# Performance work log

Measured on AMD Instinct MI355X. Metric: run time of the kernel, lower is better.

Reference implementation:

```python
import jax, jax.numpy as jnp
import numpy as np

B, S, D, H = 2, 2048, 1024, 16
DK = D // H
DFF = 4 * D
EPS = 1e-6


def layer_norm(x, gamma, beta):
    mu = jnp.mean(x, axis=-1, keepdims=True)
    var = jnp.mean(jnp.square(x - mu), axis=-1, keepdims=True)
    return (x - mu) * jax.lax.rsqrt(var + EPS) * gamma + beta


def setup_inputs() -> dict:
    key = jax.random.key(0)
    ks = jax.random.split(key, 10)
    xavier = (6.0 / (D + D)) ** 0.5
    kaiming = (6.0 / D) ** 0.5
    kaiming2 = (6.0 / DFF) ** 0.5
    return {
        "batch_X": jax.random.normal(ks[0], (B, S, D), dtype=jnp.float32),
        "padding_mask": jax.random.randint(ks[1], (B, S), 0, 2, dtype=jnp.int32),
        "W_Q": jax.random.uniform(ks[2], (D, D), jnp.float32, -xavier, xavier),
        "W_K": jax.random.uniform(ks[3], (D, D), jnp.float32, -xavier, xavier),
        "W_V": jax.random.uniform(ks[4], (D, D), jnp.float32, -xavier, xavier),
        "W_O": jax.random.uniform(ks[5], (D, D), jnp.float32, -xavier, xavier),
        "W1": jax.random.uniform(ks[6], (D, DFF), jnp.float32, -kaiming, kaiming),
        "b1": jnp.zeros((DFF,), jnp.float32),
        "W2": jax.random.uniform(ks[7], (DFF, D), jnp.float32, -kaiming2, kaiming2),
        "b2": jnp.zeros((D,), jnp.float32),
        "gamma1": jnp.ones((D,), jnp.float32),
        "beta1": jnp.zeros((D,), jnp.float32),
        "gamma2": jnp.ones((D,), jnp.float32),
        "beta2": jnp.zeros((D,), jnp.float32),
    }


def reference(batch_X, padding_mask, W_Q, W_K, W_V, W_O, W1, b1, W2, b2,
              gamma1, beta1, gamma2, beta2):
    x = batch_X
    b, s, d = x.shape

    # --- multi-head self-attention (use_mask=False: padding mask only) ---
    q = (x @ W_Q).reshape(b, s, H, DK)
    k = (x @ W_K).reshape(b, s, H, DK)
    v = (x @ W_V).reshape(b, s, H, DK)
    scores = jnp.einsum("bqhd,bkhd->bhqk", q, k) / jnp.sqrt(jnp.float32(DK))
    # mask[b,i,j] = (padding_mask[b,i] == 0) for all j: whole query rows are
    # either fully masked (softmax -> NaN -> zeroed in the original) or
    # fully unmasked. Equivalent math: softmax then zero padded query rows.
    probs = jax.nn.softmax(scores, axis=-1)
    keep = (padding_mask != 0).astype(probs.dtype)[:, None, :, None]  # [B,1,S,1]
    probs = probs * keep
    ctx = jnp.einsum("bhqk,bkhd->bqhd", probs, v).reshape(b, s, d)
    attn_out = ctx @ W_O

    # --- residual + LN (dropout identity in eval) ---
    x = x + layer_norm(attn_out, gamma1, beta1)

    # --- FFN ---
    h = jax.nn.relu(x @ W1 + b1)
    ffn_out = h @ W2 + b2
    x = x + layer_norm(ffn_out, gamma2, beta2)
    return x
```

## Files before the change

kernel.cpp:

```cpp
#include <hip/hip_runtime.h>

#define B 2
#define S 2048
#define D 1024
#define H 16
#define DKh 64
#define DFF 4096
#define M (B*S)

typedef unsigned short u16;
typedef unsigned int u32;
typedef __attribute__((ext_vector_type(8))) short short8;
typedef __attribute__((ext_vector_type(4))) float f32x4;

__device__ __forceinline__ u16 f2bf(float f) {
  union { float f; unsigned u; } v; v.f = f;
  unsigned r = v.u + 0x7fffu + ((v.u >> 16) & 1u);
  return (u16)(r >> 16);
}

__device__ __forceinline__ u32 pkbf(float a, float b) {
  union { float f; u32 u; } ua, ub; ua.f = a; ub.f = b;
  return ((ub.u + 0x8000u) & 0xffff0000u) | ((ua.u + 0x8000u) >> 16);
}

__device__ __forceinline__ void gload16(const void* g, void* l) {
  __builtin_amdgcn_global_load_lds((const __attribute__((address_space(1))) void*)g,
                                   (__attribute__((address_space(3))) void*)l, 16, 0, 0);
}

__global__ __launch_bounds__(256) void cvtbf(const float* __restrict__ in,
                                             u16* __restrict__ out, int n4) {
  int i = blockIdx.x * 256 + threadIdx.x;
  if (i >= n4) return;
  float4 v = ((const float4*)in)[i];
  ushort4 o = make_ushort4(f2bf(v.x), f2bf(v.y), f2bf(v.z), f2bf(v.w));
  ((ushort4*)out)[i] = o;
}

__global__ __launch_bounds__(256) void tcvt(const float* __restrict__ W,
                                            u16* __restrict__ Wt, int K, int N) {
  __shared__ u16 l[64][65];
  const int n0 = blockIdx.x * 64, k0 = blockIdx.y * 64;
  const int tx = threadIdx.x & 63, ty = threadIdx.x >> 6;
#pragma unroll
  for (int j = 0; j < 16; ++j) {
    int r = j * 4 + ty;
    l[r][tx] = f2bf(W[(size_t)(k0 + r) * N + n0 + tx]);
  }
  __syncthreads();
#pragma unroll
  for (int j = 0; j < 16; ++j) {
    int r = j * 4 + ty;
    Wt[(size_t)(n0 + r) * K + k0 + tx] = l[tx][r];
  }
}

__global__ __launch_bounds__(256) void vtrans(const u16* __restrict__ V,
                                              u16* __restrict__ Vt, int ld) {
  __shared__ u16 l[64][65];
  const int s0 = blockIdx.x * 64, by = blockIdx.y;
  const int b = by >> 4, h = by & 15;
  const int tx = threadIdx.x & 63, ty = threadIdx.x >> 6;
#pragma unroll
  for (int j = 0; j < 16; ++j) {
    int r = j * 4 + ty;
    l[r][tx] = V[(size_t)(b * S + s0 + r) * ld + h * DKh + tx];
  }
  __syncthreads();
#pragma unroll
  for (int j = 0; j < 16; ++j) {
    int r = j * 4 + ty;
    Vt[(size_t)(by * 64 + r) * S + s0 + tx] = l[tx][r];
  }
}

template<int EPI, int SPLIT2>
__global__ __launch_bounds__(256) void gemm_bt(const u16* __restrict__ A,
    const u16* __restrict__ Bt, void* __restrict__ Cout,
    const float* __restrict__ bias, int Mm, int N, int Kd) {
  __shared__ u16 lA[128 * 32];
  __shared__ u16 lB[128 * 32];
  const int t = threadIdx.x;
  const int lane = t & 63, w = t >> 6;
  const int wm = w >> 1, wn = w & 1;
  const int g = lane >> 4, c = lane & 15;

  const int gx = gridDim.x, gy = gridDim.y;
  const int orig = blockIdx.y * gx + blockIdx.x;
  const int qchunk = (gx * gy) >> 3;
  const int wg = (orig & 7) * qchunk + (orig >> 3);
  const int bn0 = (wg % gx) * 128, bm0 = (wg / gx) * 128;

  const int khalf = SPLIT2 ? (Kd >> 1) : Kd;
  const int koff = SPLIT2 ? blockIdx.z * khalf : 0;
  const int nk = khalf >> 5;
  f32x4 acc[4][4] = {};

  const int srow = t >> 2;
  const int scb = (t & 3) * 8;

  auto stage = [&](int kt) {
    gload16(A + (size_t)(bm0 + srow) * Kd + koff + kt * 32 + scb, (void*)(lA + t * 8));
    gload16(A + (size_t)(bm0 + 64 + srow) * Kd + koff + kt * 32 + scb, (void*)(lA + 2048 + t * 8));
    gload16(Bt + (size_t)(bn0 + srow) * Kd + koff + kt * 32 + scb, (void*)(lB + t * 8));
    gload16(Bt + (size_t)(bn0 + 64 + srow) * Kd + koff + kt * 32 + scb, (void*)(lB + 2048 + t * 8));
  };

  stage(0);
  for (int kt = 0; kt < nk; ++kt) {
    __syncthreads();
    short8 af[4], bfr[4];
#pragma unroll
    for (int mt = 0; mt < 4; ++mt)
      af[mt] = *(const short8*)&lA[(wm * 64 + mt * 16 + c) * 32 + g * 8];
#pragma unroll
    for (int nt = 0; nt < 4; ++nt)
      bfr[nt] = *(const short8*)&lB[(wn * 64 + nt * 16 + c) * 32 + g * 8];
#pragma unroll
    for (int mt = 0; mt < 4; ++mt)
#pragma unroll
      for (int nt = 0; nt < 4; ++nt)
        acc[mt][nt] = __builtin_amdgcn_mfma_f32_16x16x32_bf16(af[mt], bfr[nt], acc[mt][nt], 0, 0, 0);
    __syncthreads();
    if (kt + 1 < nk) stage(kt + 1);
  }

  float* plane = SPLIT2 ? ((float*)Cout + (size_t)blockIdx.z * Mm * N) : (float*)Cout;
#pragma unroll
  for (int mt = 0; mt < 4; ++mt) {
#pragma unroll
    for (int nt = 0; nt < 4; ++nt) {
      const int col = bn0 + wn * 64 + nt * 16 + c;
      float bv = (EPI == 2) ? bias[col] : 0.0f;
#pragma unroll
      for (int r = 0; r < 4; ++r) {
        const int row = bm0 + wm * 64 + mt * 16 + g * 4 + r;
        float v = acc[mt][nt][r];
        if (EPI == 2) v = fmaxf(v + bv, 0.0f);
        if (EPI == 1 || SPLIT2) plane[(size_t)row * N + col] = v;
        else                    ((u16*)Cout)[(size_t)row * N + col] = f2bf(v);
      }
    }
  }
}

__global__ __launch_bounds__(256) void attn_kernel(const u16* __restrict__ Q,
    const u16* __restrict__ Kp, const u16* __restrict__ Vt,
    const int* __restrict__ mask, u16* __restrict__ Ctx, int ldq) {
  __shared__ u16 lK[2][64 * 64];
  __shared__ u16 lV[2][64 * 64];
  __shared__ u16 lP[4 * 16 * 64];
  const int t = threadIdx.x, lane = t & 63, w = t >> 6;
  const int g = lane >> 4, c = lane & 15;
  const int gx = gridDim.x;
  const int orig = blockIdx.y * gx + blockIdx.x;
  const int qchunk = (gx * gridDim.y) >> 3;
  const int wg = (orig & 7) * qchunk + (orig >> 3);
  const int bx = wg % gx, by = wg / gx;
  const int b = by >> 4, h = by & 15;
  const int q0w = bx * 64 + w * 16;
  const float SCL = 0.18033688011112042f;

  short8 qf[2];
#pragma unroll
  for (int kc = 0; kc < 2; ++kc)
    qf[kc] = *(const short8*)&Q[(size_t)(b * S + q0w + c) * ldq + h * DKh + kc * 32 + g * 8];

  float lsum = 0.0f;
  f32x4 accO[4] = {};

  auto stage = [&](int buf, int it) {
    const int kv0 = it * 64;
#pragma unroll
    for (int q = 0; q < 2; ++q) {
      int idx = q * 256 + t;
      int row = idx >> 3;
      int colb = (idx & 7) * 16;
      int scol = colb ^ ((row & 7) << 4);
      gload16(Kp + (size_t)(b * S + kv0 + row) * ldq + h * DKh + scol / 2,
              (void*)(&lK[buf][0] + idx * 8));
      gload16(Vt + (size_t)(by * 64 + row) * S + kv0 + scol / 2,
              (void*)(&lV[buf][0] + idx * 8));
    }
  };

  stage(0, 0);
  int cur = 0;
  for (int it = 0; it < S / 64; ++it) {
    __syncthreads();
    if (it + 1 < S / 64) stage(cur ^ 1, it + 1);

    f32x4 sc[4];
#pragma unroll
    for (int ct = 0; ct < 4; ++ct) {
      f32x4 z = {0.f, 0.f, 0.f, 0.f};
#pragma unroll
      for (int kc = 0; kc < 2; ++kc) {
        int row = ct * 16 + c;
        int bcol = (kc * 64 + g * 16) ^ ((row & 7) << 4);
        short8 kf = *(const short8*)&lK[cur][row * 64 + bcol / 2];
        z = __builtin_amdgcn_mfma_f32_16x16x32_bf16(kf, qf[kc], z, 0, 0, 0);
      }
      sc[ct] = z;
    }

#pragma unroll
    for (int ct = 0; ct < 4; ++ct) {
      float p0 = __builtin_amdgcn_exp2f(sc[ct][0] * SCL);
      float p1 = __builtin_amdgcn_exp2f(sc[ct][1] * SCL);
      float p2 = __builtin_amdgcn_exp2f(sc[ct][2] * SCL);
      float p3 = __builtin_amdgcn_exp2f(sc[ct][3] * SCL);
      lsum += (p0 + p1) + (p2 + p3);
      uint2 pk;
      pk.x = pkbf(p0, p1);
      pk.y = pkbf(p2, p3);
      *(uint2*)&lP[w * 1024 + c * 64 + (((ct * 32 + g * 8) ^ ((c & 7) << 4)) >> 1)] = pk;
    }

    short8 pa[2];
#pragma unroll
    for (int kc = 0; kc < 2; ++kc)
      pa[kc] = *(const short8*)&lP[w * 1024 + c * 64 + (((kc * 64 + g * 16) ^ ((c & 7) << 4)) >> 1)];
#pragma unroll
    for (int dt = 0; dt < 4; ++dt) {
#pragma unroll
      for (int kc = 0; kc < 2; ++kc) {
        int rowV = dt * 16 + c;
        int bcolV = (kc * 64 + g * 16) ^ ((rowV & 7) << 4);
        short8 vb = *(const short8*)&lV[cur][rowV * 64 + bcolV / 2];
        accO[dt] = __builtin_amdgcn_mfma_f32_16x16x32_bf16(pa[kc], vb, accO[dt], 0, 0, 0);
      }
    }
    cur ^= 1;
  }

  lsum += __shfl_xor(lsum, 16);
  lsum += __shfl_xor(lsum, 32);

#pragma unroll
  for (int r = 0; r < 4; ++r) {
    int qrow = g * 4 + r;
    float lq = __shfl(lsum, qrow);
    int q = q0w + qrow;
    int keep = mask[b * S + q];
    float inv = (keep != 0) ? (1.0f / lq) : 0.0f;
#pragma unroll
    for (int dt = 0; dt < 4; ++dt) {
      float o = accO[dt][r] * inv;
      Ctx[(size_t)(b * S + q) * D + h * DKh + dt * 16 + c] = f2bf(o);
    }
  }
}

__global__ __launch_bounds__(256) void ln_res(const float* __restrict__ Y1,
    const float* __restrict__ Y2, const float* __restrict__ bias,
    const float* __restrict__ Xres, const float* __restrict__ gamma,
    const float* __restrict__ beta, float* __restrict__ outF,
    u16* __restrict__ outB) {
  __shared__ float s1[4], s2[4];
  const int row = blockIdx.x, t = threadIdx.x;
  float4 y = ((const float4*)(Y1 + (size_t)row * D))[t];
  if (Y2) {
    const float4 y2 = ((const float4*)(Y2 + (size_t)row * D))[t];
    y.x += y2.x; y.y += y2.y; y.z += y2.z; y.w += y2.w;
  }
  if (bias) {
    const float4 bb = ((const float4*)bias)[t];
    y.x += bb.x; y.y += bb.y; y.z += bb.z; y.w += bb.w;
  }
  float sm = y.x + y.y + y.z + y.w;
  float sq = y.x * y.x + y.y * y.y + y.z * y.z + y.w * y.w;
#pragma unroll
  for (int m2 = 1; m2 <= 32; m2 <<= 1) { sm += __shfl_xor(sm, m2); sq += __shfl_xor(sq, m2); }
  if ((t & 63) == 0) { s1[t >> 6] = sm; s2[t >> 6] = sq; }
  __syncthreads();
  float tot = s1[0] + s1[1] + s1[2] + s1[3];
  float tsq = s2[0] + s2[1] + s2[2] + s2[3];
  float mu = tot * (1.0f / D);
  float var = tsq * (1.0f / D) - mu * mu;
  float rstd = rsqrtf(var + 1e-6f);
  const float4 xr = ((const float4*)(Xres + (size_t)row * D))[t];
  const float4 ga = ((const float4*)gamma)[t];
  const float4 be = ((const float4*)beta)[t];
  float4 o;
  o.x = xr.x + (y.x - mu) * rstd * ga.x + be.x;
  o.y = xr.y + (y.y - mu) * rstd * ga.y + be.y;
  o.z = xr.z + (y.z - mu) * rstd * ga.z + be.z;
  o.w = xr.w + (y.w - mu) * rstd * ga.w + be.w;
  ((float4*)(outF + (size_t)row * D))[t] = o;
  if (outB) {
    ushort4 ob = make_ushort4(f2bf(o.x), f2bf(o.y), f2bf(o.z), f2bf(o.w));
    ((ushort4*)outB)[(size_t)row * (D / 4) + t] = ob;
  }
}

extern "C" void kernel_launch(void* const* d_in, const int* in_sizes, int n_in,
                              void* d_out, int out_size, void* d_ws, size_t ws_size,
                              hipStream_t stream) {
  const float* X   = (const float*)d_in[0];
  const int*   msk = (const int*)d_in[1];
  const float* WQ  = (const float*)d_in[2];
  const float* WK  = (const float*)d_in[3];
  const float* WV  = (const float*)d_in[4];
  const float* WO  = (const float*)d_in[5];
  const float* W1  = (const float*)d_in[6];
  const float* b1  = (const float*)d_in[7];
  const float* W2  = (const float*)d_in[8];
  const float* b2  = (const float*)d_in[9];
  const float* g1  = (const float*)d_in[10];
  const float* be1 = (const float*)d_in[11];
  const float* g2  = (const float*)d_in[12];
  const float* be2 = (const float*)d_in[13];
  float* out = (float*)d_out;

  char* ws = (char*)d_ws;
  size_t off = 0;
  auto alloc = [&](size_t bytes) {
    void* p = ws + off;
    off += (bytes + 1023) & ~(size_t)1023;
    return p;
  };
  u16* Xb     = (u16*)alloc((size_t)M * D * 2);
  u16* WQKVt  = (u16*)alloc((size_t)3 * D * D * 2);
  u16* WOt    = (u16*)alloc((size_t)D * D * 2);
  u16* W1t    = (u16*)alloc((size_t)DFF * D * 2);
  u16* W2t    = (u16*)alloc((size_t)D * DFF * 2);
  u16* QKVb   = (u16*)alloc((size_t)M * 3 * D * 2);
  u16* Vt     = (u16*)alloc((size_t)B * H * DKh * S * 2);
  u16* Ctx    = (u16*)alloc((size_t)M * D * 2);
  float* X1f  = (float*)alloc((size_t)M * D * 4);
  u16* X1b    = (u16*)alloc((size_t)M * D * 2);
  u16* Hb     = (u16*)alloc((size_t)M * DFF * 2);
  float* PP   = (float*)QKVb;
  if (off > ws_size) return;

  dim3 blk(256);

  cvtbf<<<dim3(M * D / 4 / 256), blk, 0, stream>>>(X, Xb, M * D / 4);
  tcvt<<<dim3(D / 64, D / 64), blk, 0, stream>>>(WQ, WQKVt + 0 * D * D, D, D);
  tcvt<<<dim3(D / 64, D / 64), blk, 0, stream>>>(WK, WQKVt + 1 * D * D, D, D);
  tcvt<<<dim3(D / 64, D / 64), blk, 0, stream>>>(WV, WQKVt + 2 * D * D, D, D);
  tcvt<<<dim3(D / 64, D / 64), blk, 0, stream>>>(WO, WOt, D, D);
  tcvt<<<dim3(DFF / 64, D / 64), blk, 0, stream>>>(W1, W1t, D, DFF);
  tcvt<<<dim3(D / 64, DFF / 64), blk, 0, stream>>>(W2, W2t, DFF, D);
  gemm_bt<0, 0><<<dim3(3 * D / 128, M / 128), blk, 0, stream>>>(Xb, WQKVt, QKVb, nullptr, M, 3 * D, D);
  vtrans<<<dim3(S / 64, B * H), blk, 0, stream>>>(QKVb + 2 * D, Vt, 3 * D);
  attn_kernel<<<dim3(S / 64, B * H), blk, 0, stream>>>(QKVb, QKVb + D, Vt, msk, Ctx, 3 * D);
  gemm_bt<1, 1><<<dim3(D / 128, M / 128, 2), blk, 0, stream>>>(Ctx, WOt, PP, nullptr, M, D, D);
  ln_res<<<dim3(M), blk, 0, stream>>>(PP, PP + (size_t)M * D, nullptr, X, g1, be1, X1f, X1b);
  gemm_bt<2, 0><<<dim3(DFF / 128, M / 128), blk, 0, stream>>>(X1b, W1t, Hb, b1, M, DFF, D);
  gemm_bt<1, 1><<<dim3(D / 128, M / 128, 2), blk, 0, stream>>>(Hb, W2t, PP, nullptr, M, D, DFF);
  ln_res<<<dim3(M), blk, 0, stream>>>(PP, PP + (size_t)M * D, b2, X1f, g2, be2, out, nullptr);
}
```

Baseline: 296.3 us.

## Replace 128x128 GEMM with 256x256 ping-pong pipelined 512-thread GEMM

Replaces the single-buffered 128x128x32 bf16 GEMM with a 256x256x64 tile kernel that uses 8 waves, double-buffered LDS filled by global_load_lds, XOR-swizzled LDS addressing and a hand-scheduled quadrant loop interleaving loads with MFMA under explicit barriers and priority hints. The aim is to hide global-load latency, raise per-block data reuse and avoid LDS bank conflicts. The FFN down-projection also switches to a 4-way K split when workspace allows, and the LN kernel now sums a variable number of partial planes. This adds 128KB of LDS per block, more partial-sum traffic, and fragile hand-tuned vmcnt waits.

```diff
diff --git a/kernel.cpp b/kernel.cpp
--- a/kernel.cpp
+++ b/kernel.cpp
@@ -29,6 +29,9 @@
                                    (__attribute__((address_space(3))) void*)l, 16, 0, 0);
 }
 
+#define SBAR()  __builtin_amdgcn_sched_barrier(0)
+#define WBAR()  __builtin_amdgcn_s_barrier()
+
 __global__ __launch_bounds__(256) void cvtbf(const float* __restrict__ in,
                                              u16* __restrict__ out, int n4) {
   int i = blockIdx.x * 256 + threadIdx.x;
@@ -75,71 +78,122 @@
   }
 }
 
-template<int EPI, int SPLIT2>
-__global__ __launch_bounds__(256) void gemm_bt(const u16* __restrict__ A,
-    const u16* __restrict__ Bt, void* __restrict__ Cout,
-    const float* __restrict__ bias, int Mm, int N, int Kd) {
-  __shared__ u16 lA[128 * 32];
-  __shared__ u16 lB[128 * 32];
+template<int EPI>
+__global__ __launch_bounds__(512, 2) void gemm256(const u16* __restrict__ Ag,
+    const u16* __restrict__ Bg, void* __restrict__ Cout,
+    const float* __restrict__ bias, int Mm, int N, int ld, int Kper) {
+  __shared__ u16 lA[2 * 16384];
+  __shared__ u16 lB[2 * 16384];
   const int t = threadIdx.x;
   const int lane = t & 63, w = t >> 6;
-  const int wm = w >> 1, wn = w & 1;
+  const int wm = w >> 2, wn = w & 3;
   const int g = lane >> 4, c = lane & 15;
+  const int swz = (c & 7) << 4;
 
   const int gx = gridDim.x, gy = gridDim.y;
   const int orig = blockIdx.y * gx + blockIdx.x;
   const int qchunk = (gx * gy) >> 3;
   const int wg = (orig & 7) * qchunk + (orig >> 3);
-  const int bn0 = (wg % gx) * 128, bm0 = (wg / gx) * 128;
-
-  const int khalf = SPLIT2 ? (Kd >> 1) : Kd;
-  const int koff = SPLIT2 ? blockIdx.z * khalf : 0;
-  const int nk = khalf >> 5;
-  f32x4 acc[4][4] = {};
-
-  const int srow = t >> 2;
-  const int scb = (t & 3) * 8;
-
-  auto stage = [&](int kt) {
-    gload16(A + (size_t)(bm0 + srow) * Kd + koff + kt * 32 + scb, (void*)(lA + t * 8));
-    gload16(A + (size_t)(bm0 + 64 + srow) * Kd + koff + kt * 32 + scb, (void*)(lA + 2048 + t * 8));
-    gload16(Bt + (size_t)(bn0 + srow) * Kd + koff + kt * 32 + scb, (void*)(lB + t * 8));
-    gload16(Bt + (size_t)(bn0 + 64 + srow) * Kd + koff + kt * 32 + scb, (void*)(lB + 2048 + t * 8));
+  const int bn0 = (wg % gx) * 256, bm0 = (wg / gx) * 256;
+  const int koff = blockIdx.z * Kper;
+  const int nk = Kper >> 6;
+
+  f32x4 acc[8][4] = {};
+  short8 af[4][2], bf[2][2];
+
+  auto stageA = [&](int h, int buf, int kt) {
+#pragma unroll
+    for (int i = 0; i < 2; ++i) {
+      int chunk = i * 512 + t;
+      int rh = chunk >> 3;
+      int cb = (chunk & 7) * 16;
+      int r = (rh & 63) + (h + 2 * (rh >> 6)) * 64;
+      gload16(Ag + (size_t)(bm0 + r) * ld + koff + kt * 64 + ((cb ^ ((r & 7) << 4)) >> 1),
+              (void*)((char*)lA + buf * 32768 + h * 16384 + chunk * 16));
+    }
   };
-
-  stage(0);
+  auto stageB = [&](int h, int buf, int kt) {
+#pragma unroll
+    for (int i = 0; i < 2; ++i) {
+      int chunk = i * 512 + t;
+      int rh = chunk >> 3;
+      int cb = (chunk & 7) * 16;
+      int r = (rh & 31) + (h + 2 * (rh >> 5)) * 32;
+      gload16(Bg + (size_t)(bn0 + r) * ld + koff + kt * 64 + ((cb ^ ((r & 7) << 4)) >> 1),
+              (void*)((char*)lB + buf * 32768 + h * 16384 + chunk * 16));
+    }
+  };
+
+#define RDA(mh) { const char* lab = (const char*)lA + cur * 32768;                          \
+  _Pragma("unroll") for (int mt2 = 0; mt2 < 4; ++mt2)                                       \
+    _Pragma("unroll") for (int kc = 0; kc < 2; ++kc)                                        \
+      af[mt2][kc] = *(const short8*)(lab + (wm * 64 + (mh) * 128 + mt2 * 16 + c) * 128      \
+                                         + ((kc * 64 + g * 16) ^ swz)); }
+#define RDB(nh) { const char* lbb = (const char*)lB + cur * 32768;                          \
+  _Pragma("unroll") for (int nt2 = 0; nt2 < 2; ++nt2)                                       \
+    _Pragma("unroll") for (int kc = 0; kc < 2; ++kc)                                        \
+      bf[nt2][kc] = *(const short8*)(lbb + ((nh) * 128 + wn * 32 + nt2 * 16 + c) * 128      \
+                                         + ((kc * 64 + g * 16) ^ swz)); }
+#define QMFMA(mh, nh) { __builtin_amdgcn_s_setprio(1);                                      \
+  _Pragma("unroll") for (int mt2 = 0; mt2 < 4; ++mt2)                                       \
+    _Pragma("unroll") for (int nt2 = 0; nt2 < 2; ++nt2)                                     \
+      _Pragma("unroll") for (int kc = 0; kc < 2; ++kc)                                      \
+        acc[(mh) * 4 + mt2][(nh) * 2 + nt2] = __builtin_amdgcn_mfma_f32_16x16x32_bf16(      \
+            af[mt2][kc], bf[nt2][kc], acc[(mh) * 4 + mt2][(nh) * 2 + nt2], 0, 0, 0);        \
+  __builtin_amdgcn_s_setprio(0); }
+
+  stageA(0, 0, 0); stageB(0, 0, 0); stageA(1, 0, 0); stageB(1, 0, 0);
+  asm volatile("s_waitcnt vmcnt(4)" ::: "memory");
+  SBAR(); WBAR(); SBAR();
+
+  int cur = 0;
   for (int kt = 0; kt < nk; ++kt) {
-    __syncthreads();
-    short8 af[4], bfr[4];
-#pragma unroll
-    for (int mt = 0; mt < 4; ++mt)
-      af[mt] = *(const short8*)&lA[(wm * 64 + mt * 16 + c) * 32 + g * 8];
-#pragma unroll
-    for (int nt = 0; nt < 4; ++nt)
-      bfr[nt] = *(const short8*)&lB[(wn * 64 + nt * 16 + c) * 32 + g * 8];
-#pragma unroll
-    for (int mt = 0; mt < 4; ++mt)
-#pragma unroll
-      for (int nt = 0; nt < 4; ++nt)
-        acc[mt][nt] = __builtin_amdgcn_mfma_f32_16x16x32_bf16(af[mt], bfr[nt], acc[mt][nt], 0, 0, 0);
-    __syncthreads();
-    if (kt + 1 < nk) stage(kt + 1);
-  }
-
-  float* plane = SPLIT2 ? ((float*)Cout + (size_t)blockIdx.z * Mm * N) : (float*)Cout;
-#pragma unroll
-  for (int mt = 0; mt < 4; ++mt) {
+    const bool more = (kt + 1 < nk);
+    RDB(0); RDA(0);
+    if (more) { stageA(0, cur ^ 1, kt + 1);
+                asm volatile("s_waitcnt vmcnt(4)" ::: "memory"); }
+    else      { asm volatile("s_waitcnt vmcnt(2)" ::: "memory"); }
+    SBAR(); WBAR(); SBAR();
+    QMFMA(0, 0);
+    SBAR(); WBAR(); SBAR();
+    RDA(1);
+    if (more) { stageB(0, cur ^ 1, kt + 1);
+                asm volatile("s_waitcnt vmcnt(4)" ::: "memory"); }
+    else      { asm volatile("s_waitcnt vmcnt(0)" ::: "memory"); }
+    SBAR(); WBAR(); SBAR();
+    QMFMA(1, 0);
+    SBAR(); WBAR(); SBAR();
+    RDB(1);
+    if (more) stageA(1, cur ^ 1, kt + 1);
+    SBAR(); WBAR(); SBAR();
+    QMFMA(1, 1);
+    SBAR(); WBAR(); SBAR();
+    RDA(0);
+    if (more) { stageB(1, cur ^ 1, kt + 1);
+                asm volatile("s_waitcnt vmcnt(4)" ::: "memory"); }
+    SBAR(); WBAR(); SBAR();
+    QMFMA(0, 1);
+    SBAR(); WBAR(); SBAR();
+    cur ^= 1;
+  }
+#undef RDA
+#undef RDB
+#undef QMFMA
+
+  float* plane = (EPI == 1) ? ((float*)Cout + (size_t)blockIdx.z * Mm * N) : (float*)Cout;
+#pragma unroll
+  for (int mt = 0; mt < 8; ++mt) {
 #pragma unroll
     for (int nt = 0; nt < 4; ++nt) {
       const int col = bn0 + wn * 64 + nt * 16 + c;
       float bv = (EPI == 2) ? bias[col] : 0.0f;
 #pragma unroll
       for (int r = 0; r < 4; ++r) {
-        const int row = bm0 + wm * 64 + mt * 16 + g * 4 + r;
+        const int row = bm0 + wm * 128 + mt * 16 + g * 4 + r;
         float v = acc[mt][nt][r];
         if (EPI == 2) v = fmaxf(v + bv, 0.0f);
-        if (EPI == 1 || SPLIT2) plane[(size_t)row * N + col] = v;
-        else                    ((u16*)Cout)[(size_t)row * N + col] = f2bf(v);
+        if (EPI == 1) plane[(size_t)row * N + col] = v;
+        else          ((u16*)Cout)[(size_t)row * N + col] = f2bf(v);
       }
     }
   }
@@ -253,16 +307,15 @@
   }
 }
 
-__global__ __launch_bounds__(256) void ln_res(const float* __restrict__ Y1,
-    const float* __restrict__ Y2, const float* __restrict__ bias,
-    const float* __restrict__ Xres, const float* __restrict__ gamma,
-    const float* __restrict__ beta, float* __restrict__ outF,
-    u16* __restrict__ outB) {
+__global__ __launch_bounds__(256) void ln_res(const float* __restrict__ planes,
+    int np, const float* __restrict__ bias, const float* __restrict__ Xres,
+    const float* __restrict__ gamma, const float* __restrict__ beta,
+    float* __restrict__ outF, u16* __restrict__ outB) {
   __shared__ float s1[4], s2[4];
   const int row = blockIdx.x, t = threadIdx.x;
-  float4 y = ((const float4*)(Y1 + (size_t)row * D))[t];
-  if (Y2) {
-    const float4 y2 = ((const float4*)(Y2 + (size_t)row * D))[t];
+  float4 y = ((const float4*)(planes + (size_t)row * D))[t];
+  for (int j = 1; j < np; ++j) {
+    const float4 y2 = ((const float4*)(planes + (size_t)j * M * D + (size_t)row * D))[t];
     y.x += y2.x; y.y += y2.y; y.z += y2.z; y.w += y2.w;
   }
   if (bias) {
@@ -334,8 +387,12 @@
   u16* Hb     = (u16*)alloc((size_t)M * DFF * 2);
   float* PP   = (float*)QKVb;
   if (off > ws_size) return;
-
-  dim3 blk(256);
+  size_t off4 = off;
+  float* PP4 = (float*)(ws + off4);
+  off4 += (size_t)4 * M * D * 4;
+  const bool split4 = (off4 <= ws_size);
+
+  dim3 blk(256), blk5(512);
 
   cvtbf<<<dim3(M * D / 4 / 256), blk, 0, stream>>>(X, Xb, M * D / 4);
   tcvt<<<dim3(D / 64, D / 64), blk, 0, stream>>>(WQ, WQKVt + 0 * D * D, D, D);
@@ -344,12 +401,17 @@
   tcvt<<<dim3(D / 64, D / 64), blk, 0, stream>>>(WO, WOt, D, D);
   tcvt<<<dim3(DFF / 64, D / 64), blk, 0, stream>>>(W1, W1t, D, DFF);
   tcvt<<<dim3(D / 64, DFF / 64), blk, 0, stream>>>(W2, W2t, DFF, D);
-  gemm_bt<0, 0><<<dim3(3 * D / 128, M / 128), blk, 0, stream>>>(Xb, WQKVt, QKVb, nullptr, M, 3 * D, D);
+  gemm256<0><<<dim3(3 * D / 256, M / 256), blk5, 0, stream>>>(Xb, WQKVt, QKVb, nullptr, M, 3 * D, D, D);
   vtrans<<<dim3(S / 64, B * H), blk, 0, stream>>>(QKVb + 2 * D, Vt, 3 * D);
   attn_kernel<<<dim3(S / 64, B * H), blk, 0, stream>>>(QKVb, QKVb + D, Vt, msk, Ctx, 3 * D);
-  gemm_bt<1, 1><<<dim3(D / 128, M / 128, 2), blk, 0, stream>>>(Ctx, WOt, PP, nullptr, M, D, D);
-  ln_res<<<dim3(M), blk, 0, stream>>>(PP, PP + (size_t)M * D, nullptr, X, g1, be1, X1f, X1b);
-  gemm_bt<2, 0><<<dim3(DFF / 128, M / 128), blk, 0, stream>>>(X1b, W1t, Hb, b1, M, DFF, D);
-  gemm_bt<1, 1><<<dim3(D / 128, M / 128, 2), blk, 0, stream>>>(Hb, W2t, PP, nullptr, M, D, DFF);
-  ln_res<<<dim3(M), blk, 0, stream>>>(PP, PP + (size_t)M * D, b2, X1f, g2, be2, out, nullptr);
-}
+  gemm256<1><<<dim3(D / 256, M / 256, 2), blk5, 0, stream>>>(Ctx, WOt, PP, nullptr, M, D, D, D / 2);
+  ln_res<<<dim3(M), blk, 0, stream>>>(PP, 2, nullptr, X, g1, be1, X1f, X1b);
+  gemm256<2><<<dim3(DFF / 256, M / 256), blk5, 0, stream>>>(X1b, W1t, Hb, b1, M, DFF, D, D);
+  if (split4) {
+    gemm256<1><<<dim3(D / 256, M / 256, 4), blk5, 0, stream>>>(Hb, W2t, PP4, nullptr, M, D, DFF, DFF / 4);
+    ln_res<<<dim3(M), blk, 0, stream>>>(PP4, 4, b2, X1f, g2, be2, out, nullptr);
+  } else {
+    gemm256<1><<<dim3(D / 256, M / 256, 2), blk5, 0, stream>>>(Hb, W2t, PP, nullptr, M, D, DFF, DFF / 2);
+    ln_res<<<dim3(M), blk, 0, stream>>>(PP, 2, b2, X1f, g2, be2, out, nullptr);
+  }
+}
```

After: 265.6 us. 10.3% less time.
